# Optimization experiments

Measured on AMD Instinct MI355X. Metric: run time of the kernel, lower is better.

## Reference

```python
import jax, jax.numpy as jnp
import numpy as np

B, L, D, E, H = 4, 2048, 512, 8, 1024

def setup_inputs() -> dict:
    key = jax.random.key(0)
    k1, k2, k3, k4 = jax.random.split(key, 4)
    x = jax.random.normal(k1, (B, L, D), dtype=jnp.float32)
    weights = jax.random.uniform(k2, (B, L, E), dtype=jnp.float32)
    w1 = jax.random.normal(k3, (E, D, H), dtype=jnp.float32) * 0.02
    b1 = jnp.zeros((E, H), dtype=jnp.float32)
    w2 = jax.random.normal(k4, (E, H, D), dtype=jnp.float32) * 0.02
    b2 = jnp.zeros((E, D), dtype=jnp.float32)
    return {"x": x, "weights": weights, "w1": w1, "b1": b1, "w2": w2, "b2": b2}

def reference(x, weights, w1, b1, w2, b2):
    # h: [B, L, E, H]
    h = jnp.einsum('bld,edh->bleh', x, w1) + b1[None, None, :, :]
    h = jax.nn.gelu(h, approximate=False)  # torch F.gelu default is exact (erf)
    # out: [B, L, E, D]
    out = jnp.einsum('bleh,ehd->bled', h, w2) + b2[None, None, :, :]
    # weighted sum over experts -> [B, L, D]
    return jnp.einsum('bled,ble->bld', out, weights)
```

## Files before the change

kernel.cpp:

```cpp
#include <hip/hip_runtime.h>
#include <hip/hip_bf16.h>

#define DEV __device__ __forceinline__

typedef __bf16 bf16;
typedef __bf16 bf16x4 __attribute__((ext_vector_type(4)));
typedef __bf16 bf16x8 __attribute__((ext_vector_type(8)));
typedef float f32x4 __attribute__((ext_vector_type(4)));

static constexpr int Bb = 4, Ll = 2048, Dd = 512, Ee = 8, Hh = 1024;
static constexpr int Mm = Bb * Ll;
static constexpr int GKS = Ee * Hh;

DEV void gload_lds16(const void* g, void* l) {
  __builtin_amdgcn_global_load_lds(
      (const __attribute__((address_space(1))) unsigned int*)g,
      (__attribute__((address_space(3))) unsigned int*)l, 16, 0, 0);
}

DEV float gelu_fast(float h) {
  const float k = 0.7978845608028654f * 2.0f * 1.4426950408889634f;
  float h2 = h * h;
  float y = h * (k + (0.044715f * k) * h2);
  float t = exp2f(y);
  return h - h * __frcp_rn(t + 1.0f);
}

__global__ void cvt_x_kernel(const float* __restrict__ in, bf16* __restrict__ out, int n4) {
  int i = blockIdx.x * blockDim.x + threadIdx.x;
  if (i < n4) {
    float4 v = ((const float4*)in)[i];
    bf16x4 o = {(bf16)v.x, (bf16)v.y, (bf16)v.z, (bf16)v.w};
    ((bf16x4*)out)[i] = o;
  }
}

__global__ void transpose_cvt(const float* __restrict__ in, bf16* __restrict__ out,
                              int R, int C, size_t in_es, size_t out_es, int out_rs) {
  __shared__ float tile[64][65];
  const int e = blockIdx.z;
  const float* ip = in + (size_t)e * in_es;
  bf16* op = out + (size_t)e * out_es;
  const int r0 = blockIdx.y * 64, c0 = blockIdx.x * 64;
  const int tc = threadIdx.x & 63, tr = threadIdx.x >> 6;
#pragma unroll
  for (int i = 0; i < 16; ++i) {
    const int r = tr + i * 4;
    tile[r][tc] = ip[(size_t)(r0 + r) * C + c0 + tc];
  }
  __syncthreads();
  const int wr = threadIdx.x & 63, wc0 = threadIdx.x >> 6;
#pragma unroll
  for (int i = 0; i < 16; ++i) {
    const int c = wc0 + i * 4;
    op[(size_t)(c0 + c) * out_rs + r0 + wr] = (bf16)tile[wr][c];
  }
}

#define PIPE_DECLS                                                   \
  const int t = threadIdx.x;                                         \
  const int lane = t & 63;                                           \
  const int wid = t >> 6;                                            \
  const int wm = wid >> 2, wn = wid & 3;                             \
  const int fr = lane & 15, fg = lane >> 4, fq = lane >> 4;          \
  const int srow = t >> 2;                                           \
  const int sq = (t & 3) ^ ((t >> 3) & 3);                           \
  const int rsl = fg ^ ((fr >> 1) & 3);

#define PHASE0(buf)                                                  \
  bf16x8 bfr[4], af[4];                                              \
  _Pragma("unroll") for (int fj = 0; fj < 4; ++fj) {                 \
    const int row = wn * 64 + fj * 16 + fr;                          \
    bfr[fj] = *(const bf16x8*)((buf) + 16384 + row * 64 + rsl * 16); \
  }                                                                  \
  _Pragma("unroll") for (int fi = 0; fi < 4; ++fi) {                 \
    const int row = wm * 128 + fi * 16 + fr;                         \
    af[fi] = *(const bf16x8*)((buf) + row * 64 + rsl * 16);          \
  }

#define PHASE1_READS(buf)                                            \
  bf16x8 af2[4];                                                     \
  _Pragma("unroll") for (int fi = 0; fi < 4; ++fi) {                 \
    const int row = wm * 128 + (4 + fi) * 16 + fr;                   \
    af2[fi] = *(const bf16x8*)((buf) + row * 64 + rsl * 16);         \
  }

#define MFMA_CLUSTER(A, ACCOFF)                                      \
  __builtin_amdgcn_s_barrier();                                      \
  asm volatile("s_waitcnt lgkmcnt(0)" ::: "memory");                 \
  __builtin_amdgcn_sched_barrier(0);                                 \
  __builtin_amdgcn_s_setprio(1);                                     \
  _Pragma("unroll") for (int fi = 0; fi < 4; ++fi)                   \
  _Pragma("unroll") for (int fj = 0; fj < 4; ++fj)                   \
    acc[(ACCOFF) + fi][fj] = __builtin_amdgcn_mfma_f32_16x16x32_bf16(\
        bfr[fj], (A)[fi], acc[(ACCOFF) + fi][fj], 0, 0, 0);          \
  __builtin_amdgcn_s_setprio(0);

__global__ __launch_bounds__(512, 1) void ffn_stage1_f(
    const bf16* __restrict__ xb, const bf16* __restrict__ w1t,
    const float* __restrict__ b1, const float* __restrict__ wts,
    bf16* __restrict__ G) {
  __shared__ __align__(16) char lds[98304];
  __shared__ float b1s[1024];
  __shared__ float wls[256];
  const int mt = blockIdx.x, e = blockIdx.y;
  PIPE_DECLS
  b1s[t] = b1[e * Hh + t];
  b1s[512 + t] = b1[e * Hh + 512 + t];
  if (t < 256) wls[t] = wts[((size_t)mt * 256 + t) * Ee + e];

  const bf16* Ag = xb + (size_t)mt * 256 * Dd;
  const bf16* Bg0 = w1t + (size_t)e * Hh * Dd;

  auto stageA = [&](int it, char* buf) {
    const int k0 = (it & 15) * 32;
    gload_lds16(Ag + (size_t)srow * Dd + k0 + sq * 8, buf + wid * 1024);
    gload_lds16(Ag + (size_t)(128 + srow) * Dd + k0 + sq * 8, buf + 8192 + wid * 1024);
  };
  auto stageB = [&](int it, char* buf) {
    const bf16* Bg = Bg0 + (size_t)(it >> 4) * 256 * Dd;
    const int k0 = (it & 15) * 32;
    gload_lds16(Bg + (size_t)srow * Dd + k0 + sq * 8, buf + 16384 + wid * 1024);
    gload_lds16(Bg + (size_t)(128 + srow) * Dd + k0 + sq * 8, buf + 24576 + wid * 1024);
  };

  f32x4 acc[8][4] = {};
  const int NT = 64;
  stageA(0, lds); stageB(0, lds);
  stageA(1, lds + 32768); stageB(1, lds + 32768);
  for (int it = 0; it < NT; ++it) {
    char* buf = lds + (it % 3) * 32768;
    char* nbuf = lds + ((it + 2) % 3) * 32768;
    if (it + 1 < NT) {
      asm volatile("s_waitcnt vmcnt(4)" ::: "memory");
    } else {
      asm volatile("s_waitcnt vmcnt(0)" ::: "memory");
    }
    __builtin_amdgcn_s_barrier();
    {
      PHASE0(buf)
      if (it + 2 < NT) stageA(it + 2, nbuf);
      MFMA_CLUSTER(af, 0)
      PHASE1_READS(buf)
      if (it + 2 < NT) stageB(it + 2, nbuf);
      MFMA_CLUSTER(af2, 4)
    }
    if ((it & 15) == 15) {
      const int ct = it >> 4;
      float b1v[4][4];
#pragma unroll
      for (int fj = 0; fj < 4; ++fj)
#pragma unroll
        for (int r = 0; r < 4; ++r)
          b1v[fj][r] = b1s[ct * 256 + wn * 64 + fj * 16 + fq * 4 + r];
#pragma unroll
      for (int fi = 0; fi < 8; ++fi) {
        const int m = mt * 256 + wm * 128 + fi * 16 + fr;
        const float wgt = wls[wm * 128 + fi * 16 + fr];
        bf16* gp = G + (size_t)m * GKS + e * Hh + ct * 256 + wn * 64 + fq * 4;
#pragma unroll
        for (int fj = 0; fj < 4; ++fj) {
          bf16x4 o;
#pragma unroll
          for (int r = 0; r < 4; ++r) {
            float v = acc[fi][fj][r] + b1v[fj][r];
            o[r] = (bf16)(gelu_fast(v) * wgt);
          }
          *(bf16x4*)(gp + fj * 16) = o;
#pragma unroll
          for (int r = 0; r < 4; ++r) acc[fi][fj][r] = 0.f;
        }
      }
    }
  }
}

__global__ __launch_bounds__(512, 1) void ffn_stage2_f(
    const bf16* __restrict__ G, const bf16* __restrict__ w2t,
    float* __restrict__ P) {
  __shared__ __align__(16) char lds[98304];
  const int mt = blockIdx.x, nt = blockIdx.y, s = blockIdx.z;
  PIPE_DECLS
  const bf16* Ag = G + (size_t)mt * 256 * GKS + (size_t)s * 2048;
  const bf16* Bg = w2t + (size_t)nt * 256 * GKS + (size_t)s * 2048;

  auto stageA = [&](int it, char* buf) {
    const int k0 = it * 32;
    gload_lds16(Ag + (size_t)srow * GKS + k0 + sq * 8, buf + wid * 1024);
    gload_lds16(Ag + (size_t)(128 + srow) * GKS + k0 + sq * 8, buf + 8192 + wid * 1024);
  };
  auto stageB = [&](int it, char* buf) {
    const int k0 = it * 32;
    gload_lds16(Bg + (size_t)srow * GKS + k0 + sq * 8, buf + 16384 + wid * 1024);
    gload_lds16(Bg + (size_t)(128 + srow) * GKS + k0 + sq * 8, buf + 24576 + wid * 1024);
  };

  f32x4 acc[8][4] = {};
  const int NT = 64;
  stageA(0, lds); stageB(0, lds);
  stageA(1, lds + 32768); stageB(1, lds + 32768);
  for (int it = 0; it < NT; ++it) {
    char* buf = lds + (it % 3) * 32768;
    char* nbuf = lds + ((it + 2) % 3) * 32768;
    if (it + 1 < NT) {
      asm volatile("s_waitcnt vmcnt(4)" ::: "memory");
    } else {
      asm volatile("s_waitcnt vmcnt(0)" ::: "memory");
    }
    __builtin_amdgcn_s_barrier();
    {
      PHASE0(buf)
      if (it + 2 < NT) stageA(it + 2, nbuf);
      MFMA_CLUSTER(af, 0)
      PHASE1_READS(buf)
      if (it + 2 < NT) stageB(it + 2, nbuf);
      MFMA_CLUSTER(af2, 4)
    }
  }

  float* Pp = P + (size_t)s * Mm * Dd;
#pragma unroll
  for (int fi = 0; fi < 8; ++fi) {
    const size_t m = (size_t)mt * 256 + wm * 128 + fi * 16 + fr;
    float* pp = Pp + m * Dd + nt * 256 + wn * 64 + fq * 4;
#pragma unroll
    for (int fj = 0; fj < 4; ++fj) *(f32x4*)(pp + fj * 16) = acc[fi][fj];
  }
}

__global__ __launch_bounds__(256) void reduce_bias(
    const float* __restrict__ P, const float* __restrict__ wts,
    const float* __restrict__ b2, float* __restrict__ out, int S) {
  const int n4 = Mm * Dd / 4;
  int i = blockIdx.x * 256 + threadIdx.x;
  if (i >= n4) return;
  const int m = i / (Dd / 4);
  const int d0 = (i % (Dd / 4)) * 4;
  float4 a = ((const float4*)P)[i];
  for (int s = 1; s < S; ++s) {
    float4 p = ((const float4*)P)[(size_t)s * n4 + i];
    a.x += p.x; a.y += p.y; a.z += p.z; a.w += p.w;
  }
  const float* wr = wts + (size_t)m * Ee;
#pragma unroll
  for (int e = 0; e < Ee; ++e) {
    const float w = wr[e];
    float4 b = *(const float4*)(b2 + e * Dd + d0);
    a.x += w * b.x; a.y += w * b.y; a.z += w * b.z; a.w += w * b.w;
  }
  ((float4*)out)[i] = a;
}

template <int ARS, int BRS>
DEV void gemm_core(const bf16* __restrict__ Ag, const bf16* __restrict__ Bg,
                   int ksteps, f32x4 (&acc)[4][4], bf16* As, bf16* Bs) {
  const int t = threadIdx.x;
  const int lane = t & 63;
  const int w = t >> 6;
  const int srow = t >> 3;
  const int sseg = t & 7;
  const int wr = w >> 1, wc = w & 1;
  const int fr = lane & 15;
  const int fg = lane >> 4;
  for (int s = 0; s < ksteps; ++s) {
    __syncthreads();
#pragma unroll
    for (int i = 0; i < 4; ++i) {
      const int row = i * 32 + srow;
      const int q = sseg ^ (row & 7);
      gload_lds16(Ag + (size_t)row * ARS + s * 64 + q * 8,
                  (char*)As + i * 4096 + w * 1024);
      gload_lds16(Bg + (size_t)row * BRS + s * 64 + q * 8,
                  (char*)Bs + i * 4096 + w * 1024);
    }
    __syncthreads();
#pragma unroll
    for (int kk = 0; kk < 2; ++kk) {
      bf16x8 af[4], bfr[4];
#pragma unroll
      for (int mi = 0; mi < 4; ++mi) {
        const int row = wr * 64 + mi * 16 + fr;
        const int q = (kk * 4 + fg) ^ (row & 7);
        af[mi] = *(const bf16x8*)((const char*)As + row * 128 + q * 16);
      }
#pragma unroll
      for (int ni = 0; ni < 4; ++ni) {
        const int row = wc * 64 + ni * 16 + fr;
        const int q = (kk * 4 + fg) ^ (row & 7);
        bfr[ni] = *(const bf16x8*)((const char*)Bs + row * 128 + q * 16);
      }
#pragma unroll
      for (int mi = 0; mi < 4; ++mi)
#pragma unroll
        for (int ni = 0; ni < 4; ++ni)
          acc[mi][ni] = __builtin_amdgcn_mfma_f32_16x16x32_bf16(
              af[mi], bfr[ni], acc[mi][ni], 0, 0, 0);
    }
  }
}

__global__ __launch_bounds__(256) void ffn_stage1_t(
    const bf16* __restrict__ xb, const bf16* __restrict__ w1t,
    const float* __restrict__ b1, const float* __restrict__ wts,
    bf16* __restrict__ G) {
  __shared__ __align__(16) bf16 As[128 * 64];
  __shared__ __align__(16) bf16 Bs[128 * 64];
  __shared__ float b1s[128];
  __shared__ float wls[128];
  const int mt = blockIdx.x, ht = blockIdx.y, e = blockIdx.z;
  const int t = threadIdx.x;
  if (t < 128) b1s[t] = b1[e * Hh + ht * 128 + t];
  else wls[t - 128] = wts[((size_t)mt * 128 + (t - 128)) * Ee + e];
  f32x4 acc[4][4] = {};
  const bf16* Ag = xb + (size_t)mt * 128 * Dd;
  const bf16* Bg = w1t + ((size_t)e * Hh + (size_t)ht * 128) * Dd;
  gemm_core<Dd, Dd>(Ag, Bg, Dd / 64, acc, As, Bs);
  const int lane = t & 63, w = t >> 6;
  const int wr = w >> 1, wc = w & 1, fr = lane & 15, fq = lane >> 4;
  float bcol[4];
#pragma unroll
  for (int ni = 0; ni < 4; ++ni) bcol[ni] = b1s[wc * 64 + ni * 16 + fr];
  bf16* gp = G + ((size_t)mt * 128 + wr * 64 + fq * 4) * GKS
               + (size_t)e * Hh + ht * 128 + wc * 64 + fr;
#pragma unroll
  for (int mi = 0; mi < 4; ++mi)
#pragma unroll
    for (int r = 0; r < 4; ++r) {
      const float wgt = wls[wr * 64 + mi * 16 + fq * 4 + r];
#pragma unroll
      for (int ni = 0; ni < 4; ++ni) {
        float v = acc[mi][ni][r] + bcol[ni];
        gp[(size_t)(mi * 16 + r) * GKS + ni * 16] = (bf16)(gelu_fast(v) * wgt);
      }
    }
}

__global__ __launch_bounds__(256) void ffn_stage2_partial(
    const bf16* __restrict__ G, const bf16* __restrict__ w2t,
    float* __restrict__ P, int kchunk) {
  __shared__ __align__(16) bf16 As[128 * 64];
  __shared__ __align__(16) bf16 Bs[128 * 64];
  const int mt = blockIdx.x, nt = blockIdx.y, s = blockIdx.z;
  f32x4 acc[4][4] = {};
  const bf16* Ag = G + (size_t)mt * 128 * GKS + (size_t)s * kchunk;
  const bf16* Bg = w2t + (size_t)nt * 128 * GKS + (size_t)s * kchunk;
  gemm_core<GKS, GKS>(Ag, Bg, kchunk / 64, acc, As, Bs);
  float* Pp = P + (size_t)s * Mm * Dd;
  const int t = threadIdx.x;
  const int lane = t & 63, w = t >> 6;
  const int wr = w >> 1, wc = w & 1, fr = lane & 15, fq = lane >> 4;
#pragma unroll
  for (int mi = 0; mi < 4; ++mi)
#pragma unroll
    for (int r = 0; r < 4; ++r) {
      const size_t m = (size_t)mt * 128 + wr * 64 + mi * 16 + fq * 4 + r;
#pragma unroll
      for (int ni = 0; ni < 4; ++ni) {
        const int d = nt * 128 + wc * 64 + ni * 16 + fr;
        Pp[m * Dd + d] = acc[mi][ni][r];
      }
    }
}

extern "C" void kernel_launch(void* const* d_in, const int* in_sizes, int n_in,
                              void* d_out, int out_size, void* d_ws, size_t ws_size,
                              hipStream_t stream) {
  const float* x   = (const float*)d_in[0];
  const float* wts = (const float*)d_in[1];
  const float* w1  = (const float*)d_in[2];
  const float* b1  = (const float*)d_in[3];
  const float* w2  = (const float*)d_in[4];
  const float* b2  = (const float*)d_in[5];
  float* out = (float*)d_out;

  char* ws = (char*)d_ws;
  size_t off = 0;
  bf16* xb  = (bf16*)(ws + off); off += (size_t)Mm * Dd * 2;
  bf16* w1t = (bf16*)(ws + off); off += (size_t)Ee * Hh * Dd * 2;
  bf16* w2t = (bf16*)(ws + off); off += (size_t)Dd * Ee * Hh * 2;

  const size_t gfull = (size_t)Mm * Ee * Hh * 2;
  const size_t psz   = (size_t)Mm * Dd * 4;

  cvt_x_kernel<<<(Mm * Dd / 4 + 255) / 256, 256, 0, stream>>>(x, xb, Mm * Dd / 4);
  transpose_cvt<<<dim3(Hh / 64, Dd / 64, Ee), 256, 0, stream>>>(
      w1, w1t, Dd, Hh, (size_t)Dd * Hh, (size_t)Hh * Dd, Dd);
  transpose_cvt<<<dim3(Dd / 64, Hh / 64, Ee), 256, 0, stream>>>(
      w2, w2t, Hh, Dd, (size_t)Hh * Dd, (size_t)Hh, Ee * Hh);

  if (ws_size >= off + gfull + 4 * psz) {
    bf16* G = (bf16*)(ws + off);
    float* P = (float*)(ws + off + gfull);
    ffn_stage1_f<<<dim3(Mm / 256, Ee), 512, 0, stream>>>(
        xb, w1t, b1, wts, G);
    ffn_stage2_f<<<dim3(Mm / 256, Dd / 256, 4), 512, 0, stream>>>(
        G, w2t, P);
    reduce_bias<<<(Mm * Dd / 4 + 255) / 256, 256, 0, stream>>>(P, wts, b2, out, 4);
  } else if (ws_size >= off + gfull + 2 * psz) {
    bf16* G = (bf16*)(ws + off);
    float* P = (float*)(ws + off + gfull);
    ffn_stage1_t<<<dim3(Mm / 128, Hh / 128, Ee), 256, 0, stream>>>(
        xb, w1t, b1, wts, G);
    ffn_stage2_partial<<<dim3(Mm / 128, Dd / 128, 2), 256, 0, stream>>>(
        G, w2t, P, GKS / 2);
    reduce_bias<<<(Mm * Dd / 4 + 255) / 256, 256, 0, stream>>>(P, wts, b2, out, 2);
  }
}
```

Measured before the change: 223.9 us.

## Store intermediate G in contiguous 256x256 tiles and unify stage-2 path

Stage 1 now writes the gelu-weighted intermediate as contiguous 256x256 bf16 tiles indexed by (expert, m-tile, h-tile) instead of row-major rows with a 16 KB stride. Stage 2 reads A from those tiles, so each row's load covers 512 contiguous bytes rather than striding across the full GKS row. This is meant to improve DRAM/TLB locality for the intermediate. The fallback 128-tile kernels are removed and the split count S is passed as a parameter to the fast path.

```diff
diff --git a/kernel.cpp b/kernel.cpp
--- a/kernel.cpp
+++ b/kernel.cpp
@@ -11,6 +11,7 @@
 static constexpr int Bb = 4, Ll = 2048, Dd = 512, Ee = 8, Hh = 1024;
 static constexpr int Mm = Bb * Ll;
 static constexpr int GKS = Ee * Hh;
+static constexpr int TSZ = 65536;
 
 DEV void gload_lds16(const void* g, void* l) {
   __builtin_amdgcn_global_load_lds(
@@ -147,6 +148,7 @@
     }
     if ((it & 15) == 15) {
       const int ct = it >> 4;
+      bf16* tbase = G + ((((size_t)e * 32 + mt) * 4) + ct) * TSZ;
       float b1v[4][4];
 #pragma unroll
       for (int fj = 0; fj < 4; ++fj)
@@ -155,9 +157,9 @@
           b1v[fj][r] = b1s[ct * 256 + wn * 64 + fj * 16 + fq * 4 + r];
 #pragma unroll
       for (int fi = 0; fi < 8; ++fi) {
-        const int m = mt * 256 + wm * 128 + fi * 16 + fr;
-        const float wgt = wls[wm * 128 + fi * 16 + fr];
-        bf16* gp = G + (size_t)m * GKS + e * Hh + ct * 256 + wn * 64 + fq * 4;
+        const int mp = wm * 128 + fi * 16 + fr;
+        const float wgt = wls[mp];
+        bf16* gp = tbase + (size_t)mp * 256 + wn * 64 + fq * 4;
 #pragma unroll
         for (int fj = 0; fj < 4; ++fj) {
           bf16x4 o;
@@ -177,17 +179,19 @@
 
 __global__ __launch_bounds__(512, 1) void ffn_stage2_f(
     const bf16* __restrict__ G, const bf16* __restrict__ w2t,
-    float* __restrict__ P) {
+    float* __restrict__ P, int eslabs) {
   __shared__ __align__(16) char lds[98304];
   const int mt = blockIdx.x, nt = blockIdx.y, s = blockIdx.z;
   PIPE_DECLS
-  const bf16* Ag = G + (size_t)mt * 256 * GKS + (size_t)s * 2048;
-  const bf16* Bg = w2t + (size_t)nt * 256 * GKS + (size_t)s * 2048;
+  const bf16* Bg = w2t + (size_t)nt * 256 * GKS + (size_t)s * eslabs * Hh;
 
   auto stageA = [&](int it, char* buf) {
-    const int k0 = it * 32;
-    gload_lds16(Ag + (size_t)srow * GKS + k0 + sq * 8, buf + wid * 1024);
-    gload_lds16(Ag + (size_t)(128 + srow) * GKS + k0 + sq * 8, buf + 8192 + wid * 1024);
+    const int eidx = s * eslabs + (it >> 5);
+    const int ct = (it >> 3) & 3;
+    const int hp = (it & 7) * 32;
+    const bf16* tb = G + ((((size_t)eidx * 32 + mt) * 4) + ct) * TSZ;
+    gload_lds16(tb + (size_t)srow * 256 + hp + sq * 8, buf + wid * 1024);
+    gload_lds16(tb + (size_t)(128 + srow) * 256 + hp + sq * 8, buf + 8192 + wid * 1024);
   };
   auto stageB = [&](int it, char* buf) {
     const int k0 = it * 32;
@@ -196,7 +200,7 @@
   };
 
   f32x4 acc[8][4] = {};
-  const int NT = 64;
+  const int NT = eslabs * 32;
   stageA(0, lds); stageB(0, lds);
   stageA(1, lds + 32768); stageB(1, lds + 32768);
   for (int it = 0; it < NT; ++it) {
@@ -251,117 +255,6 @@
   ((float4*)out)[i] = a;
 }
 
-template <int ARS, int BRS>
-DEV void gemm_core(const bf16* __restrict__ Ag, const bf16* __restrict__ Bg,
-                   int ksteps, f32x4 (&acc)[4][4], bf16* As, bf16* Bs) {
-  const int t = threadIdx.x;
-  const int lane = t & 63;
-  const int w = t >> 6;
-  const int srow = t >> 3;
-  const int sseg = t & 7;
-  const int wr = w >> 1, wc = w & 1;
-  const int fr = lane & 15;
-  const int fg = lane >> 4;
-  for (int s = 0; s < ksteps; ++s) {
-    __syncthreads();
-#pragma unroll
-    for (int i = 0; i < 4; ++i) {
-      const int row = i * 32 + srow;
-      const int q = sseg ^ (row & 7);
-      gload_lds16(Ag + (size_t)row * ARS + s * 64 + q * 8,
-                  (char*)As + i * 4096 + w * 1024);
-      gload_lds16(Bg + (size_t)row * BRS + s * 64 + q * 8,
-                  (char*)Bs + i * 4096 + w * 1024);
-    }
-    __syncthreads();
-#pragma unroll
-    for (int kk = 0; kk < 2; ++kk) {
-      bf16x8 af[4], bfr[4];
-#pragma unroll
-      for (int mi = 0; mi < 4; ++mi) {
-        const int row = wr * 64 + mi * 16 + fr;
-        const int q = (kk * 4 + fg) ^ (row & 7);
-        af[mi] = *(const bf16x8*)((const char*)As + row * 128 + q * 16);
-      }
-#pragma unroll
-      for (int ni = 0; ni < 4; ++ni) {
-        const int row = wc * 64 + ni * 16 + fr;
-        const int q = (kk * 4 + fg) ^ (row & 7);
-        bfr[ni] = *(const bf16x8*)((const char*)Bs + row * 128 + q * 16);
-      }
-#pragma unroll
-      for (int mi = 0; mi < 4; ++mi)
-#pragma unroll
-        for (int ni = 0; ni < 4; ++ni)
-          acc[mi][ni] = __builtin_amdgcn_mfma_f32_16x16x32_bf16(
-              af[mi], bfr[ni], acc[mi][ni], 0, 0, 0);
-    }
-  }
-}
-
-__global__ __launch_bounds__(256) void ffn_stage1_t(
-    const bf16* __restrict__ xb, const bf16* __restrict__ w1t,
-    const float* __restrict__ b1, const float* __restrict__ wts,
-    bf16* __restrict__ G) {
-  __shared__ __align__(16) bf16 As[128 * 64];
-  __shared__ __align__(16) bf16 Bs[128 * 64];
-  __shared__ float b1s[128];
-  __shared__ float wls[128];
-  const int mt = blockIdx.x, ht = blockIdx.y, e = blockIdx.z;
-  const int t = threadIdx.x;
-  if (t < 128) b1s[t] = b1[e * Hh + ht * 128 + t];
-  else wls[t - 128] = wts[((size_t)mt * 128 + (t - 128)) * Ee + e];
-  f32x4 acc[4][4] = {};
-  const bf16* Ag = xb + (size_t)mt * 128 * Dd;
-  const bf16* Bg = w1t + ((size_t)e * Hh + (size_t)ht * 128) * Dd;
-  gemm_core<Dd, Dd>(Ag, Bg, Dd / 64, acc, As, Bs);
-  const int lane = t & 63, w = t >> 6;
-  const int wr = w >> 1, wc = w & 1, fr = lane & 15, fq = lane >> 4;
-  float bcol[4];
-#pragma unroll
-  for (int ni = 0; ni < 4; ++ni) bcol[ni] = b1s[wc * 64 + ni * 16 + fr];
-  bf16* gp = G + ((size_t)mt * 128 + wr * 64 + fq * 4) * GKS
-               + (size_t)e * Hh + ht * 128 + wc * 64 + fr;
-#pragma unroll
-  for (int mi = 0; mi < 4; ++mi)
-#pragma unroll
-    for (int r = 0; r < 4; ++r) {
-      const float wgt = wls[wr * 64 + mi * 16 + fq * 4 + r];
-#pragma unroll
-      for (int ni = 0; ni < 4; ++ni) {
-        float v = acc[mi][ni][r] + bcol[ni];
-        gp[(size_t)(mi * 16 + r) * GKS + ni * 16] = (bf16)(gelu_fast(v) * wgt);
-      }
-    }
-}
-
-__global__ __launch_bounds__(256) void ffn_stage2_partial(
-    const bf16* __restrict__ G, const bf16* __restrict__ w2t,
-    float* __restrict__ P, int kchunk) {
-  __shared__ __align__(16) bf16 As[128 * 64];
-  __shared__ __align__(16) bf16 Bs[128 * 64];
-  const int mt = blockIdx.x, nt = blockIdx.y, s = blockIdx.z;
-  f32x4 acc[4][4] = {};
-  const bf16* Ag = G + (size_t)mt * 128 * GKS + (size_t)s * kchunk;
-  const bf16* Bg = w2t + (size_t)nt * 128 * GKS + (size_t)s * kchunk;
-  gemm_core<GKS, GKS>(Ag, Bg, kchunk / 64, acc, As, Bs);
-  float* Pp = P + (size_t)s * Mm * Dd;
-  const int t = threadIdx.x;
-  const int lane = t & 63, w = t >> 6;
-  const int wr = w >> 1, wc = w & 1, fr = lane & 15, fq = lane >> 4;
-#pragma unroll
-  for (int mi = 0; mi < 4; ++mi)
-#pragma unroll
-    for (int r = 0; r < 4; ++r) {
-      const size_t m = (size_t)mt * 128 + wr * 64 + mi * 16 + fq * 4 + r;
-#pragma unroll
-      for (int ni = 0; ni < 4; ++ni) {
-        const int d = nt * 128 + wc * 64 + ni * 16 + fr;
-        Pp[m * Dd + d] = acc[mi][ni][r];
-      }
-    }
-}
-
 extern "C" void kernel_launch(void* const* d_in, const int* in_sizes, int n_in,
                               void* d_out, int out_size, void* d_ws, size_t ws_size,
                               hipStream_t stream) {
@@ -388,21 +281,17 @@
   transpose_cvt<<<dim3(Dd / 64, Hh / 64, Ee), 256, 0, stream>>>(
       w2, w2t, Hh, Dd, (size_t)Hh * Dd, (size_t)Hh, Ee * Hh);
 
-  if (ws_size >= off + gfull + 4 * psz) {
+  int S = 0;
+  if (ws_size >= off + gfull + 4 * psz) S = 4;
+  else if (ws_size >= off + gfull + 2 * psz) S = 2;
+
+  if (S >= 2) {
     bf16* G = (bf16*)(ws + off);
     float* P = (float*)(ws + off + gfull);
     ffn_stage1_f<<<dim3(Mm / 256, Ee), 512, 0, stream>>>(
         xb, w1t, b1, wts, G);
-    ffn_stage2_f<<<dim3(Mm / 256, Dd / 256, 4), 512, 0, stream>>>(
-        G, w2t, P);
-    reduce_bias<<<(Mm * Dd / 4 + 255) / 256, 256, 0, stream>>>(P, wts, b2, out, 4);
-  } else if (ws_size >= off + gfull + 2 * psz) {
-    bf16* G = (bf16*)(ws + off);
-    float* P = (float*)(ws + off + gfull);
-    ffn_stage1_t<<<dim3(Mm / 128, Hh / 128, Ee), 256, 0, stream>>>(
-        xb, w1t, b1, wts, G);
-    ffn_stage2_partial<<<dim3(Mm / 128, Dd / 128, 2), 256, 0, stream>>>(
-        G, w2t, P, GKS / 2);
-    reduce_bias<<<(Mm * Dd / 4 + 255) / 256, 256, 0, stream>>>(P, wts, b2, out, 2);
-  }
-}
+    ffn_stage2_f<<<dim3(Mm / 256, Dd / 256, S), 512, 0, stream>>>(
+        G, w2t, P, Ee / S);
+    reduce_bias<<<(Mm * Dd / 4 + 255) / 256, 256, 0, stream>>>(P, wts, b2, out, S);
+  }
+}
```

After: 225.1 us. About the same (+0.5%).
